# Optimization experiments

Hardware: AMD Instinct MI355X
Metric: run time of the kernel (lower is better)

Reference implementation:

```python
import jax, jax.numpy as jnp
import numpy as np

B, T, I, H, L = 64, 2048, 512, 512, 2


def setup_inputs() -> dict:
    key = jax.random.key(0)
    ks = jax.random.split(key, 9)
    inp = {"x": jax.random.normal(ks[0], (B, T, I), dtype=jnp.float32)}
    names = ["w_ih_0", "w_hh_0", "b_ih_0", "b_hh_0", "w_ih_1", "w_hh_1", "b_ih_1", "b_hh_1"]
    shapes = [(I, H), (H, H), (H,), (H,), (H, H), (H, H), (H,), (H,)]
    for n, s, k in zip(names, shapes, ks[1:]):
        scale = 0.1 if n.startswith("w") else 1.0
        inp[n] = jax.random.uniform(k, s, dtype=jnp.float32) * scale
    return inp


def reference(x, w_ih_0, w_hh_0, b_ih_0, b_hh_0, w_ih_1, w_hh_1, b_ih_1, b_hh_1):
    # params per layer: (w_ih, w_hh, b) with b = b_ih + b_hh fused
    params = [(w_ih_0, w_hh_0, b_ih_0 + b_hh_0), (w_ih_1, w_hh_1, b_ih_1 + b_hh_1)]
    batch = x.shape[0]
    h0 = jnp.zeros((L, batch, H), dtype=x.dtype)
    x_tm = jnp.swapaxes(x, 0, 1)  # [T, B, I] time-major for scan

    def step(h, x_t):
        new_h = []
        inp = x_t
        for layer in range(L):
            w_ih, w_hh, b = params[layer]
            h_new = jnp.tanh(inp @ w_ih + h[layer] @ w_hh + b)
            new_h.append(h_new)
            inp = h_new
        return jnp.stack(new_h, axis=0), new_h[-1]

    final_h, out_tm = jax.lax.scan(step, h0, x_tm)
    output = jnp.swapaxes(out_tm, 0, 1)  # [B, T, H]
    return output, final_h
```

## Files before the change

### kernel.cpp

```cpp
#include <hip/hip_runtime.h>
#include <stdint.h>


#define BDIM 64
#define TDIM 2048
#define IDIM 512
#define HDIM 512

#define NBLK 32
#define NA   16
#define CPB  32
#define BH   (BDIM * HDIM)

typedef float f32x4 __attribute__((ext_vector_type(4)));
typedef __bf16 bf16x8 __attribute__((ext_vector_type(8)));

__device__ __forceinline__ float fast_tanh(float z) {
    float e = __expf(2.0f * z);
    return 1.0f - 2.0f / (e + 1.0f);
}

__global__ __launch_bounds__(256, 2) void xw0_gemm(
    const float* __restrict__ x, const float* __restrict__ wih0,
    float* __restrict__ pre) {
    const int nt = blockIdx.x & 15;
    const int mt = blockIdx.x >> 4;
    const int c0 = nt * 32;
    const int tx = threadIdx.x, lane = tx & 63, wv = tx >> 6;

    __shared__ __bf16 WH[16 * 2 * 64 * 8];
    __shared__ __bf16 WL[16 * 2 * 64 * 8];
    for (int e = tx; e < 16 * 2 * 64; e += 256) {
        int kk = e >> 7, t = (e >> 6) & 1, l = e & 63;
        int kbase = kk * 32 + ((l >> 4) << 3);
        int col = c0 + t * 16 + (l & 15);
        bf16x8 vh, vl;
#pragma unroll
        for (int j = 0; j < 8; ++j) {
            float w = wih0[(size_t)(kbase + j) * HDIM + col];
            __bf16 hi = (__bf16)w;
            vh[j] = hi; vl[j] = (__bf16)(w - (float)hi);
        }
        *reinterpret_cast<bf16x8*>(&WH[e * 8]) = vh;
        *reinterpret_cast<bf16x8*>(&WL[e * 8]) = vl;
    }
    __syncthreads();

    const int kfo = (lane >> 4) << 3;
    const int rbase = mt * 256 + wv * 64;
    const int rA = lane & 15;
    f32x4 acc[4][2];
#pragma unroll
    for (int rt = 0; rt < 4; ++rt) {
        acc[rt][0] = {0.f, 0.f, 0.f, 0.f};
        acc[rt][1] = {0.f, 0.f, 0.f, 0.f};
    }
#pragma unroll 2
    for (int kk = 0; kk < 16; ++kk) {
        bf16x8 w0h = *reinterpret_cast<const bf16x8*>(&WH[((kk * 2 + 0) * 64 + lane) * 8]);
        bf16x8 w1h = *reinterpret_cast<const bf16x8*>(&WH[((kk * 2 + 1) * 64 + lane) * 8]);
        bf16x8 w0l = *reinterpret_cast<const bf16x8*>(&WL[((kk * 2 + 0) * 64 + lane) * 8]);
        bf16x8 w1l = *reinterpret_cast<const bf16x8*>(&WL[((kk * 2 + 1) * 64 + lane) * 8]);
#pragma unroll
        for (int rt = 0; rt < 4; ++rt) {
            const float* xr = x + (size_t)(rbase + rt * 16 + rA) * IDIM + kk * 32 + kfo;
            f32x4 l4 = *reinterpret_cast<const f32x4*>(xr);
            f32x4 h4 = *reinterpret_cast<const f32x4*>(xr + 4);
            bf16x8 xh, xl;
#pragma unroll
            for (int j = 0; j < 4; ++j) {
                __bf16 a = (__bf16)l4[j]; xh[j] = a;     xl[j] = (__bf16)(l4[j] - (float)a);
                __bf16 b = (__bf16)h4[j]; xh[4 + j] = b; xl[4 + j] = (__bf16)(h4[j] - (float)b);
            }
            acc[rt][0] = __builtin_amdgcn_mfma_f32_16x16x32_bf16(xh, w0h, acc[rt][0], 0, 0, 0);
            acc[rt][1] = __builtin_amdgcn_mfma_f32_16x16x32_bf16(xh, w1h, acc[rt][1], 0, 0, 0);
            acc[rt][0] = __builtin_amdgcn_mfma_f32_16x16x32_bf16(xl, w0h, acc[rt][0], 0, 0, 0);
            acc[rt][1] = __builtin_amdgcn_mfma_f32_16x16x32_bf16(xl, w1h, acc[rt][1], 0, 0, 0);
            acc[rt][0] = __builtin_amdgcn_mfma_f32_16x16x32_bf16(xh, w0l, acc[rt][0], 0, 0, 0);
            acc[rt][1] = __builtin_amdgcn_mfma_f32_16x16x32_bf16(xh, w1l, acc[rt][1], 0, 0, 0);
        }
    }
    const int rowOff = (lane >> 4) << 2, colL = lane & 15;
#pragma unroll
    for (int rt = 0; rt < 4; ++rt)
#pragma unroll
        for (int ct = 0; ct < 2; ++ct)
#pragma unroll
            for (int m = 0; m < 4; ++m)
                __builtin_nontemporal_store(acc[rt][ct][m],
                    &pre[(size_t)(rbase + rt * 16 + rowOff + m) * HDIM + c0 + ct * 16 + colL]);
}

__global__ __launch_bounds__(256, 1) void rnn_persistent(
    const float* __restrict__ whh0,
    const float* __restrict__ bih0, const float* __restrict__ bhh0,
    const float* __restrict__ wih1, const float* __restrict__ whh1,
    const float* __restrict__ bih1, const float* __restrict__ bhh1,
    float* out, unsigned char* __restrict__ ws) {

    unsigned* flags = (unsigned*)ws;
    __bf16* h0base  = (__bf16*)(ws + 4096);
    __bf16* h1base  = (__bf16*)(ws + 4096 + 4 * (size_t)(2 * BH) * 2);

    const int blk  = blockIdx.x;
    const bool isA = (blk < NA);
    const int c0   = (isA ? blk : blk - NA) * CPB;
    const int tx   = threadIdx.x;
    const int lane = tx & 63;
    const int wv   = tx >> 6;
    const int r0   = wv * 16;

    __shared__ __bf16 WH[32 * 2 * 64 * 8];
    __shared__ __bf16 WL[32 * 2 * 64 * 8];
    {
        const int ne = (isA ? 16 : 32) * 2 * 64;
        const float* W1 = isA ? whh0 : wih1;
        for (int e = tx; e < ne; e += 256) {
            int kk = e >> 7, t = (e >> 6) & 1, l = e & 63;
            int kbase = kk * 32 + ((l >> 4) << 3);
            int col = c0 + t * 16 + (l & 15);
            bf16x8 vh, vl;
#pragma unroll
            for (int j = 0; j < 8; ++j) {
                int kidx = kbase + j;
                float w = (kidx < 512) ? W1[(size_t)kidx * HDIM + col]
                                       : whh1[(size_t)(kidx - 512) * HDIM + col];
                __bf16 hi = (__bf16)w;
                vh[j] = hi; vl[j] = (__bf16)(w - (float)hi);
            }
            *reinterpret_cast<bf16x8*>(&WH[e * 8]) = vh;
            *reinterpret_cast<bf16x8*>(&WL[e * 8]) = vl;
        }
    }
    const int colD = c0 + (lane & 15);
    const int rowD = r0 + ((lane >> 4) << 2);
    const int rA   = r0 + (lane & 15);
    const int kfo  = (lane >> 4) << 3;
    const float bias0 = isA ? (bih0[colD] + bhh0[colD]) : (bih1[colD] + bhh1[colD]);
    const float bias1 = isA ? (bih0[colD + 16] + bhh0[colD + 16])
                            : (bih1[colD + 16] + bhh1[colD + 16]);
    __syncthreads();

    auto hhalf_mfma = [&](const __bf16* hi_row, const __bf16* lo_row, int koff,
                          f32x4& a0, f32x4& a1) {
#pragma unroll
        for (int kk = 0; kk < 16; ++kk) {
            bf16x8 hh = *reinterpret_cast<const bf16x8*>(hi_row + kk * 32 + kfo);
            bf16x8 w0h = *reinterpret_cast<const bf16x8*>(&WH[(((koff + kk) * 2 + 0) * 64 + lane) * 8]);
            bf16x8 w1h = *reinterpret_cast<const bf16x8*>(&WH[(((koff + kk) * 2 + 1) * 64 + lane) * 8]);
            bf16x8 w0l = *reinterpret_cast<const bf16x8*>(&WL[(((koff + kk) * 2 + 0) * 64 + lane) * 8]);
            bf16x8 w1l = *reinterpret_cast<const bf16x8*>(&WL[(((koff + kk) * 2 + 1) * 64 + lane) * 8]);
            a0 = __builtin_amdgcn_mfma_f32_16x16x32_bf16(hh, w0h, a0, 0, 0, 0);
            a1 = __builtin_amdgcn_mfma_f32_16x16x32_bf16(hh, w1h, a1, 0, 0, 0);
            a0 = __builtin_amdgcn_mfma_f32_16x16x32_bf16(hh, w0l, a0, 0, 0, 0);
            a1 = __builtin_amdgcn_mfma_f32_16x16x32_bf16(hh, w1l, a1, 0, 0, 0);
        }
#pragma unroll
        for (int kk = 0; kk < 16; ++kk) {
            bf16x8 hl = *reinterpret_cast<const bf16x8*>(lo_row + kk * 32 + kfo);
            bf16x8 w0h = *reinterpret_cast<const bf16x8*>(&WH[(((koff + kk) * 2 + 0) * 64 + lane) * 8]);
            bf16x8 w1h = *reinterpret_cast<const bf16x8*>(&WH[(((koff + kk) * 2 + 1) * 64 + lane) * 8]);
            a0 = __builtin_amdgcn_mfma_f32_16x16x32_bf16(hl, w0h, a0, 0, 0, 0);
            a1 = __builtin_amdgcn_mfma_f32_16x16x32_bf16(hl, w1h, a1, 0, 0, 0);
        }
    };

    f32x4 pa0, pa1;
    if (isA) {
#pragma unroll
        for (int m = 0; m < 4; ++m) {
            pa0[m] = __builtin_nontemporal_load(
                &out[((size_t)(rowD + m) * TDIM + 0) * HDIM + colD]);
            pa1[m] = __builtin_nontemporal_load(
                &out[((size_t)(rowD + m) * TDIM + 0) * HDIM + colD + 16]);
        }
    }

    float vout[2][4];

    for (int k = 0; k <= TDIM; ++k) {
        if (isA && k < TDIM) {
            const __bf16* hs = h0base + ((k + 3) & 3) * (2 * BH);
            f32x4 acc0 = pa0, acc1 = pa1;
            hhalf_mfma(hs + rA * HDIM, hs + BH + rA * HDIM, 0, acc0, acc1);
            __bf16* hd = h0base + (k & 3) * (2 * BH);
#pragma unroll
            for (int m = 0; m < 4; ++m) {
                float v0 = fast_tanh(acc0[m] + bias0);
                float v1 = fast_tanh(acc1[m] + bias1);
                __bf16 a = (__bf16)v0, b = (__bf16)v1;
                hd[(rowD + m) * HDIM + colD] = a;
                hd[(rowD + m) * HDIM + colD + 16] = b;
                hd[BH + (rowD + m) * HDIM + colD] = (__bf16)(v0 - (float)a);
                hd[BH + (rowD + m) * HDIM + colD + 16] = (__bf16)(v1 - (float)b);
                if (k == TDIM - 1) {
                    out[(size_t)BDIM * TDIM * HDIM + (size_t)(rowD + m) * HDIM + colD] = v0;
                    out[(size_t)BDIM * TDIM * HDIM + (size_t)(rowD + m) * HDIM + colD + 16] = v1;
                }
            }
        } else if (!isA && k >= 1) {
            const __bf16* s0 = h0base + ((k + 3) & 3) * (2 * BH);
            const __bf16* s1 = h1base + (k & 1) * (2 * BH);
            f32x4 acc0 = {0.f, 0.f, 0.f, 0.f}, acc1 = {0.f, 0.f, 0.f, 0.f};
            hhalf_mfma(s1 + rA * HDIM, s1 + BH + rA * HDIM, 16, acc0, acc1);
            hhalf_mfma(s0 + rA * HDIM, s0 + BH + rA * HDIM, 0, acc0, acc1);
            __bf16* hd = h1base + ((k + 1) & 1) * (2 * BH);
#pragma unroll
            for (int m = 0; m < 4; ++m) {
                vout[0][m] = fast_tanh(acc0[m] + bias0);
                vout[1][m] = fast_tanh(acc1[m] + bias1);
                if (k < TDIM) {
                    __bf16 a = (__bf16)vout[0][m], b = (__bf16)vout[1][m];
                    hd[(rowD + m) * HDIM + colD] = a;
                    hd[(rowD + m) * HDIM + colD + 16] = b;
                    hd[BH + (rowD + m) * HDIM + colD] = (__bf16)(vout[0][m] - (float)a);
                    hd[BH + (rowD + m) * HDIM + colD + 16] = (__bf16)(vout[1][m] - (float)b);
                }
            }
            if (k == TDIM) {
                const int t = k - 1;
#pragma unroll
                for (int m = 0; m < 4; ++m) {
                    __builtin_nontemporal_store(vout[0][m],
                        &out[((size_t)(rowD + m) * TDIM + t) * HDIM + colD]);
                    __builtin_nontemporal_store(vout[1][m],
                        &out[((size_t)(rowD + m) * TDIM + t) * HDIM + colD + 16]);
                    out[(size_t)BDIM * TDIM * HDIM + (size_t)(BDIM + rowD + m) * HDIM + colD] = vout[0][m];
                    out[(size_t)BDIM * TDIM * HDIM + (size_t)(BDIM + rowD + m) * HDIM + colD + 16] = vout[1][m];
                }
            }
        }

        if (k < TDIM) {
            __syncthreads();
            if (tx == 0)
                __hip_atomic_store(&flags[blk * 32], (unsigned)(k + 1),
                                   __ATOMIC_RELEASE, __HIP_MEMORY_SCOPE_AGENT);
        }

        if (isA) {
            if (k + 1 < TDIM) {
#pragma unroll
                for (int m = 0; m < 4; ++m) {
                    pa0[m] = __builtin_nontemporal_load(
                        &out[((size_t)(rowD + m) * TDIM + (k + 1)) * HDIM + colD]);
                    pa1[m] = __builtin_nontemporal_load(
                        &out[((size_t)(rowD + m) * TDIM + (k + 1)) * HDIM + colD + 16]);
                }
            }
        } else if (k >= 1 && k < TDIM) {
            const int t = k - 1;
#pragma unroll
            for (int m = 0; m < 4; ++m) {
                __builtin_nontemporal_store(vout[0][m],
                    &out[((size_t)(rowD + m) * TDIM + t) * HDIM + colD]);
                __builtin_nontemporal_store(vout[1][m],
                    &out[((size_t)(rowD + m) * TDIM + t) * HDIM + colD + 16]);
            }
        }

        if (k < TDIM) {
            if (wv == 0) {
                const int fl = lane & 31;
                unsigned tgt = (unsigned)(k + 1);
                if (isA && fl >= NA) tgt = (k >= 2) ? (unsigned)(k - 2) : 0u;
                int spins = 0;
                while (true) {
                    unsigned f = __hip_atomic_load(&flags[fl * 32], __ATOMIC_RELAXED,
                                                   __HIP_MEMORY_SCOPE_AGENT);
                    if (__all((int)(f >= tgt))) break;
                    if ((++spins & 127) == 0)
                        __builtin_amdgcn_fence(__ATOMIC_ACQUIRE, "agent");
                    __builtin_amdgcn_s_sleep(1);
                }
                __builtin_amdgcn_fence(__ATOMIC_ACQUIRE, "agent");
            }
            __syncthreads();
        }
    }
}

extern "C" void kernel_launch(void* const* d_in, const int* in_sizes, int n_in,
                              void* d_out, int out_size, void* d_ws, size_t ws_size,
                              hipStream_t stream) {
    (void)in_sizes; (void)n_in; (void)out_size; (void)ws_size;
    const float* x    = (const float*)d_in[0];
    const float* wih0 = (const float*)d_in[1];
    const float* whh0 = (const float*)d_in[2];
    const float* bih0 = (const float*)d_in[3];
    const float* bhh0 = (const float*)d_in[4];
    const float* wih1 = (const float*)d_in[5];
    const float* whh1 = (const float*)d_in[6];
    const float* bih1 = (const float*)d_in[7];
    const float* bhh1 = (const float*)d_in[8];
    float* out = (float*)d_out;
    unsigned char* ws = (unsigned char*)d_ws;

    hipMemsetAsync(ws, 0, 4096 + 6 * (size_t)(2 * BDIM * HDIM * 2), stream);

    xw0_gemm<<<dim3(8192), dim3(256), 0, stream>>>(x, wih0, out);

    void* args[] = {&whh0, &bih0, &bhh0, &wih1, &whh1, &bih1, &bhh1, &out, &ws};
    hipError_t err = hipLaunchCooperativeKernel((void*)rnn_persistent, dim3(NBLK),
                                                dim3(256), args, 0, stream);
    if (err != hipSuccess) {
        rnn_persistent<<<dim3(NBLK), dim3(256), 0, stream>>>(
            whh0, bih0, bhh0, wih1, whh1, bih1, bhh1, out, ws);
    }
}
```

Measured before the change: 27.04 ms.

## Replace acquire/release fences with system-scope cache-bypassing h loads and stores

The hidden-state exchange between blocks now uses system-scope relaxed atomic loads and sc0 sc1 stores that bypass the non-coherent caches, in place of agent-scope release/acquire fences around the flag handshake. The spin-wait moves to the top of each step, and all h fragments are loaded into registers up front so loads overlap. The MFMA loop is fused into one pass over hi/lo parts. The aim is to remove the cost of the L2/L1 writeback and invalidate fences on the critical recurrent path. The risk is that memory ordering now depends on s_waitcnt plus relaxed flags, and system-scope accesses may have higher latency.

After: 33.93 ms. 25.5% more time.

```diff
diff --git a/kernel.cpp b/kernel.cpp
--- a/kernel.cpp
+++ b/kernel.cpp
@@ -11,6 +11,7 @@
 #define NA   16
 #define CPB  32
 #define BH   (BDIM * HDIM)
+#define SLOT (2 * BH)
 
 typedef float f32x4 __attribute__((ext_vector_type(4)));
 typedef __bf16 bf16x8 __attribute__((ext_vector_type(8)));
@@ -18,6 +19,21 @@
 __device__ __forceinline__ float fast_tanh(float z) {
     float e = __expf(2.0f * z);
     return 1.0f - 2.0f / (e + 1.0f);
+}
+
+__device__ __forceinline__ bf16x8 ldsys16(const __bf16* p) {
+    union { unsigned long long q[2]; bf16x8 v; } u;
+    u.q[0] = __hip_atomic_load((const unsigned long long*)p, __ATOMIC_RELAXED,
+                               __HIP_MEMORY_SCOPE_SYSTEM);
+    u.q[1] = __hip_atomic_load(((const unsigned long long*)p) + 1, __ATOMIC_RELAXED,
+                               __HIP_MEMORY_SCOPE_SYSTEM);
+    return u.v;
+}
+
+__device__ __forceinline__ void stsys_bf16(__bf16* p, float f) {
+    union { __bf16 h; unsigned short s; } c; c.h = (__bf16)f;
+    unsigned int bits = c.s;
+    asm volatile("global_store_short %0, %1, off sc0 sc1" :: "v"(p), "v"(bits));
 }
 
 __global__ __launch_bounds__(256, 2) void xw0_gemm(
@@ -100,7 +116,7 @@
 
     unsigned* flags = (unsigned*)ws;
     __bf16* h0base  = (__bf16*)(ws + 4096);
-    __bf16* h1base  = (__bf16*)(ws + 4096 + 4 * (size_t)(2 * BH) * 2);
+    __bf16* h1base  = (__bf16*)(ws + 4096 + 4 * (size_t)SLOT * 2);
 
     const int blk  = blockIdx.x;
     const bool isA = (blk < NA);
@@ -143,25 +159,23 @@
 
     auto hhalf_mfma = [&](const __bf16* hi_row, const __bf16* lo_row, int koff,
                           f32x4& a0, f32x4& a1) {
+        bf16x8 fh[16], fl[16];
+#pragma unroll
+        for (int kk = 0; kk < 16; ++kk) fh[kk] = ldsys16(hi_row + kk * 32 + kfo);
+#pragma unroll
+        for (int kk = 0; kk < 16; ++kk) fl[kk] = ldsys16(lo_row + kk * 32 + kfo);
 #pragma unroll
         for (int kk = 0; kk < 16; ++kk) {
-            bf16x8 hh = *reinterpret_cast<const bf16x8*>(hi_row + kk * 32 + kfo);
             bf16x8 w0h = *reinterpret_cast<const bf16x8*>(&WH[(((koff + kk) * 2 + 0) * 64 + lane) * 8]);
             bf16x8 w1h = *reinterpret_cast<const bf16x8*>(&WH[(((koff + kk) * 2 + 1) * 64 + lane) * 8]);
             bf16x8 w0l = *reinterpret_cast<const bf16x8*>(&WL[(((koff + kk) * 2 + 0) * 64 + lane) * 8]);
             bf16x8 w1l = *reinterpret_cast<const bf16x8*>(&WL[(((koff + kk) * 2 + 1) * 64 + lane) * 8]);
-            a0 = __builtin_amdgcn_mfma_f32_16x16x32_bf16(hh, w0h, a0, 0, 0, 0);
-            a1 = __builtin_amdgcn_mfma_f32_16x16x32_bf16(hh, w1h, a1, 0, 0, 0);
-            a0 = __builtin_amdgcn_mfma_f32_16x16x32_bf16(hh, w0l, a0, 0, 0, 0);
-            a1 = __builtin_amdgcn_mfma_f32_16x16x32_bf16(hh, w1l, a1, 0, 0, 0);
-        }
-#pragma unroll
-        for (int kk = 0; kk < 16; ++kk) {
-            bf16x8 hl = *reinterpret_cast<const bf16x8*>(lo_row + kk * 32 + kfo);
-            bf16x8 w0h = *reinterpret_cast<const bf16x8*>(&WH[(((koff + kk) * 2 + 0) * 64 + lane) * 8]);
-            bf16x8 w1h = *reinterpret_cast<const bf16x8*>(&WH[(((koff + kk) * 2 + 1) * 64 + lane) * 8]);
-            a0 = __builtin_amdgcn_mfma_f32_16x16x32_bf16(hl, w0h, a0, 0, 0, 0);
-            a1 = __builtin_amdgcn_mfma_f32_16x16x32_bf16(hl, w1h, a1, 0, 0, 0);
+            a0 = __builtin_amdgcn_mfma_f32_16x16x32_bf16(fh[kk], w0h, a0, 0, 0, 0);
+            a1 = __builtin_amdgcn_mfma_f32_16x16x32_bf16(fh[kk], w1h, a1, 0, 0, 0);
+            a0 = __builtin_amdgcn_mfma_f32_16x16x32_bf16(fl[kk], w0h, a0, 0, 0, 0);
+            a1 = __builtin_amdgcn_mfma_f32_16x16x32_bf16(fl[kk], w1h, a1, 0, 0, 0);
+            a0 = __builtin_amdgcn_mfma_f32_16x16x32_bf16(fh[kk], w0l, a0, 0, 0, 0);
+            a1 = __builtin_amdgcn_mfma_f32_16x16x32_bf16(fh[kk], w1l, a1, 0, 0, 0);
         }
     };
 
@@ -169,52 +183,67 @@
     if (isA) {
 #pragma unroll
         for (int m = 0; m < 4; ++m) {
-            pa0[m] = __builtin_nontemporal_load(
-                &out[((size_t)(rowD + m) * TDIM + 0) * HDIM + colD]);
-            pa1[m] = __builtin_nontemporal_load(
-                &out[((size_t)(rowD + m) * TDIM + 0) * HDIM + colD + 16]);
+            pa0[m] = __builtin_nontemporal_load(&out[((size_t)(rowD + m) * TDIM) * HDIM + colD]);
+            pa1[m] = __builtin_nontemporal_load(&out[((size_t)(rowD + m) * TDIM) * HDIM + colD + 16]);
         }
     }
 
     float vout[2][4];
 
     for (int k = 0; k <= TDIM; ++k) {
+        if (k > 0) {
+            if (wv == 0) {
+                const int fl = lane & 31;
+                unsigned tgt;
+                if (isA) tgt = (fl < NA) ? (unsigned)k
+                                         : (k >= 3 ? (unsigned)(k - 2) : 0u);
+                else     tgt = (unsigned)k;
+                while (true) {
+                    unsigned f = __hip_atomic_load(&flags[fl * 32], __ATOMIC_RELAXED,
+                                                   __HIP_MEMORY_SCOPE_SYSTEM);
+                    if (__all((int)(f >= tgt))) break;
+                    __builtin_amdgcn_s_sleep(1);
+                }
+            }
+            __syncthreads();
+        }
+
         if (isA && k < TDIM) {
-            const __bf16* hs = h0base + ((k + 3) & 3) * (2 * BH);
+            const __bf16* hs = h0base + ((k + 3) & 3) * SLOT;
             f32x4 acc0 = pa0, acc1 = pa1;
             hhalf_mfma(hs + rA * HDIM, hs + BH + rA * HDIM, 0, acc0, acc1);
-            __bf16* hd = h0base + (k & 3) * (2 * BH);
+            __bf16* hd = h0base + (k & 3) * SLOT;
 #pragma unroll
             for (int m = 0; m < 4; ++m) {
                 float v0 = fast_tanh(acc0[m] + bias0);
                 float v1 = fast_tanh(acc1[m] + bias1);
-                __bf16 a = (__bf16)v0, b = (__bf16)v1;
-                hd[(rowD + m) * HDIM + colD] = a;
-                hd[(rowD + m) * HDIM + colD + 16] = b;
-                hd[BH + (rowD + m) * HDIM + colD] = (__bf16)(v0 - (float)a);
-                hd[BH + (rowD + m) * HDIM + colD + 16] = (__bf16)(v1 - (float)b);
+                stsys_bf16(&hd[(rowD + m) * HDIM + colD], v0);
+                stsys_bf16(&hd[(rowD + m) * HDIM + colD + 16], v1);
+                stsys_bf16(&hd[BH + (rowD + m) * HDIM + colD], v0 - (float)(__bf16)v0);
+                stsys_bf16(&hd[BH + (rowD + m) * HDIM + colD + 16], v1 - (float)(__bf16)v1);
                 if (k == TDIM - 1) {
                     out[(size_t)BDIM * TDIM * HDIM + (size_t)(rowD + m) * HDIM + colD] = v0;
                     out[(size_t)BDIM * TDIM * HDIM + (size_t)(rowD + m) * HDIM + colD + 16] = v1;
                 }
             }
         } else if (!isA && k >= 1) {
-            const __bf16* s0 = h0base + ((k + 3) & 3) * (2 * BH);
-            const __bf16* s1 = h1base + (k & 1) * (2 * BH);
+            const __bf16* s0 = h0base + ((k + 3) & 3) * SLOT;
+            const __bf16* s1 = h1base + (k & 1) * SLOT;
             f32x4 acc0 = {0.f, 0.f, 0.f, 0.f}, acc1 = {0.f, 0.f, 0.f, 0.f};
             hhalf_mfma(s1 + rA * HDIM, s1 + BH + rA * HDIM, 16, acc0, acc1);
             hhalf_mfma(s0 + rA * HDIM, s0 + BH + rA * HDIM, 0, acc0, acc1);
-            __bf16* hd = h1base + ((k + 1) & 1) * (2 * BH);
+            __bf16* hd = h1base + ((k + 1) & 1) * SLOT;
 #pragma unroll
             for (int m = 0; m < 4; ++m) {
                 vout[0][m] = fast_tanh(acc0[m] + bias0);
                 vout[1][m] = fast_tanh(acc1[m] + bias1);
                 if (k < TDIM) {
-                    __bf16 a = (__bf16)vout[0][m], b = (__bf16)vout[1][m];
-                    hd[(rowD + m) * HDIM + colD] = a;
-                    hd[(rowD + m) * HDIM + colD + 16] = b;
-                    hd[BH + (rowD + m) * HDIM + colD] = (__bf16)(vout[0][m] - (float)a);
-                    hd[BH + (rowD + m) * HDIM + colD + 16] = (__bf16)(vout[1][m] - (float)b);
+                    stsys_bf16(&hd[(rowD + m) * HDIM + colD], vout[0][m]);
+                    stsys_bf16(&hd[(rowD + m) * HDIM + colD + 16], vout[1][m]);
+                    stsys_bf16(&hd[BH + (rowD + m) * HDIM + colD],
+                               vout[0][m] - (float)(__bf16)vout[0][m]);
+                    stsys_bf16(&hd[BH + (rowD + m) * HDIM + colD + 16],
+                               vout[1][m] - (float)(__bf16)vout[1][m]);
                 }
             }
             if (k == TDIM) {
@@ -232,10 +261,11 @@
         }
 
         if (k < TDIM) {
+            asm volatile("s_waitcnt vmcnt(0)" ::: "memory");
             __syncthreads();
             if (tx == 0)
                 __hip_atomic_store(&flags[blk * 32], (unsigned)(k + 1),
-                                   __ATOMIC_RELEASE, __HIP_MEMORY_SCOPE_AGENT);
+                                   __ATOMIC_RELAXED, __HIP_MEMORY_SCOPE_SYSTEM);
         }
 
         if (isA) {
@@ -257,25 +287,6 @@
                 __builtin_nontemporal_store(vout[1][m],
                     &out[((size_t)(rowD + m) * TDIM + t) * HDIM + colD + 16]);
             }
-        }
-
-        if (k < TDIM) {
-            if (wv == 0) {
-                const int fl = lane & 31;
-                unsigned tgt = (unsigned)(k + 1);
-                if (isA && fl >= NA) tgt = (k >= 2) ? (unsigned)(k - 2) : 0u;
-                int spins = 0;
-                while (true) {
-                    unsigned f = __hip_atomic_load(&flags[fl * 32], __ATOMIC_RELAXED,
-                                                   __HIP_MEMORY_SCOPE_AGENT);
-                    if (__all((int)(f >= tgt))) break;
-                    if ((++spins & 127) == 0)
-                        __builtin_amdgcn_fence(__ATOMIC_ACQUIRE, "agent");
-                    __builtin_amdgcn_s_sleep(1);
-                }
-                __builtin_amdgcn_fence(__ATOMIC_ACQUIRE, "agent");
-            }
-            __syncthreads();
         }
     }
 }
@@ -296,7 +307,7 @@
     float* out = (float*)d_out;
     unsigned char* ws = (unsigned char*)d_ws;
 
-    hipMemsetAsync(ws, 0, 4096 + 6 * (size_t)(2 * BDIM * HDIM * 2), stream);
+    hipMemsetAsync(ws, 0, 4096 + 6 * (size_t)SLOT * 2, stream);
 
     xw0_gemm<<<dim3(8192), dim3(256), 0, stream>>>(x, wih0, out);
 
```
